# Optimization experiments

Measured on AMD Instinct MI355X. Metric: run time of the kernel, lower is better.

The kernel has to match this reference:

```python
import jax, jax.numpy as jnp
import numpy as np

# dims: B=1, T=2048 (prefill), dim=3072, Hq=32, Hkv=8, D=128, S=max_seq_len=4096

def _rotate_interleave(x):
    # (-x1, x0, -x3, x2, ...) pairwise rotation on last dim
    x = x.reshape(x.shape[:-1] + (-1, 2))
    x = jnp.stack((-x[..., 1], x[..., 0]), axis=-1)
    return x.reshape(x.shape[:-2] + (-1,))


def setup_inputs() -> dict:
    key = jax.random.key(0)
    ks = jax.random.split(key, 8)
    B, T, DIM, HQ, HKV, HD, S = 1, 2048, 3072, 32, 8, 128, 4096
    x = jax.random.normal(ks[0], (B, T, DIM), jnp.float32)
    wq = jax.random.normal(ks[1], (HQ * HD, DIM), jnp.float32) * 0.02
    wk = jax.random.normal(ks[2], (HKV * HD, DIM), jnp.float32) * 0.02
    wv = jax.random.normal(ks[3], (HKV * HD, DIM), jnp.float32) * 0.02
    wo = jax.random.normal(ks[4], (DIM, HQ * HD), jnp.float32) * 0.02
    freqs_cos = jax.random.uniform(ks[5], (T, HD), jnp.float32)
    freqs_sin = jax.random.uniform(ks[6], (T, HD), jnp.float32)
    input_pos = jnp.zeros((1,), jnp.int32)
    k_cache = jnp.zeros((1, S, HKV, HD), jnp.float32)
    v_cache = jnp.zeros((1, S, HKV, HD), jnp.float32)
    return {"x": x, "wq": wq, "wk": wk, "wv": wv, "wo": wo,
            "freqs_cos": freqs_cos, "freqs_sin": freqs_sin,
            "k_cache": k_cache, "v_cache": v_cache, "input_pos": input_pos}


def reference(x, wq, wk, wv, wo, freqs_cos, freqs_sin, k_cache, v_cache, input_pos):
    B, T, _ = x.shape
    HQ, HKV, HD = 32, 8, 128
    q = (x @ wq.T).reshape(B, T, HQ, HD)
    k = (x @ wk.T).reshape(B, T, HKV, HD)
    v = (x @ wv.T).reshape(B, T, HKV, HD)
    # interleaved RoPE (computed in fp32 as in apply_rotary_emb)
    fc = freqs_cos[None, :, None, :]
    fs = freqs_sin[None, :, None, :]
    q = q * fc + _rotate_interleave(q) * fs
    k = k * fc + _rotate_interleave(k) * fs
    # KV-cache update at start_pos (torch.ops.llama.update_cache)
    sp = input_pos[0]
    k_all = jax.lax.dynamic_update_slice(k_cache, k, (0, sp, 0, 0))  # [1,S,HKV,HD]
    v_all = jax.lax.dynamic_update_slice(v_cache, v, (0, sp, 0, 0))
    S = k_all.shape[1]
    # GQA: expand kv heads to match q heads (head h -> kv head h // rep)
    rep = HQ // HKV
    kr = jnp.repeat(k_all, rep, axis=2)  # [1,S,HQ,HD]
    vr = jnp.repeat(v_all, rep, axis=2)
    scale = 1.0 / np.sqrt(HD).astype(np.float32)
    scores = jnp.einsum('bthd,bshd->bhts', q, kr) * scale  # [B,HQ,T,S]
    # causal mask relative to start_pos (custom_sdpa is_causal=True path)
    qpos = sp + jnp.arange(T)
    kpos = jnp.arange(S)
    mask = kpos[None, :] <= qpos[:, None]                   # [T,S]
    scores = jnp.where(mask[None, None], scores, jnp.float32(-1e30))
    attn = jax.nn.softmax(scores, axis=-1)
    y = jnp.einsum('bhts,bshd->bthd', attn, vr).reshape(B, T, HQ * HD)
    return y @ wo.T
```

## Files before the change

### kernel.cpp

```cpp
#include <hip/hip_runtime.h>
#include <hip/hip_bf16.h>
#include <stdint.h>

typedef float f32x4 __attribute__((ext_vector_type(4)));
typedef short s16x8 __attribute__((ext_vector_type(8)));
typedef short s16x4 __attribute__((ext_vector_type(4)));
typedef unsigned short u16x2 __attribute__((ext_vector_type(2)));
typedef unsigned short u16x4 __attribute__((ext_vector_type(4)));

#define AS1 __attribute__((address_space(1)))
#define AS3 __attribute__((address_space(3)))

static constexpr int T_    = 2048;
static constexpr int DIM_  = 3072;
static constexpr int HQ_   = 32;
static constexpr int HKV_  = 8;
static constexpr int HD_   = 128;
static constexpr int S_    = 4096;
static constexpr int NQKV_ = HQ_ * HD_ + 2 * HKV_ * HD_;

__device__ __forceinline__ unsigned short f2b(float f) {
  return __builtin_bit_cast(unsigned short, __float2bfloat16(f));
}
__device__ __forceinline__ float b2f(unsigned short u) {
  return __bfloat162float(__builtin_bit_cast(__hip_bfloat16, u));
}
__device__ __forceinline__ float exp2a(float x) {
  float r; asm("v_exp_f32 %0, %1" : "=v"(r) : "v"(x)); return r;
}

__device__ __forceinline__ void gld_lds16(const void* g, void* l) {
  __builtin_amdgcn_global_load_lds((AS1 unsigned int*)(uintptr_t)g,
                                   (AS3 unsigned int*)l, 16, 0, 0);
}

#define FENCE() asm volatile("" ::: "memory")
#define BAR()   do { FENCE(); __builtin_amdgcn_s_barrier(); FENCE(); } while (0)
#define WAIT_VM(n)   asm volatile("s_waitcnt vmcnt(" #n ")" ::: "memory")
#define WAIT_LGKM(n) asm volatile("s_waitcnt lgkmcnt(" #n ")" ::: "memory")
#define SCHEDB()     __builtin_amdgcn_sched_barrier(0)

__global__ __launch_bounds__(256)
void k_cvt(const float* __restrict__ src, unsigned short* __restrict__ dst, int n4) {
  int i = blockIdx.x * 256 + threadIdx.x;
  if (i >= n4) return;
  float4 v = reinterpret_cast<const float4*>(src)[i];
  u16x4 o;
  o.x = f2b(v.x); o.y = f2b(v.y); o.z = f2b(v.z); o.w = f2b(v.w);
  reinterpret_cast<u16x4*>(dst)[i] = o;
}

__global__ __launch_bounds__(256)
void k_cvtW(const float* __restrict__ wq, const float* __restrict__ wk,
            const float* __restrict__ wv, unsigned short* __restrict__ dst) {
  int idx = blockIdx.x * 256 + threadIdx.x;
  if (idx >= 4718592) return;
  const float* src; int s;
  if (idx < 3145728)      { src = wq; s = idx; }
  else if (idx < 3932160) { src = wk; s = idx - 3145728; }
  else                    { src = wv; s = idx - 3932160; }
  float4 v = reinterpret_cast<const float4*>(src)[s];
  u16x4 o;
  o.x = f2b(v.x); o.y = f2b(v.y); o.z = f2b(v.z); o.w = f2b(v.w);
  reinterpret_cast<u16x4*>(dst)[idx] = o;
}

template<int BMT, bool OUT_BF16>
__global__ __launch_bounds__(512, 4)
void k_gemm192(const unsigned short* __restrict__ A,
               const unsigned short* __restrict__ B,
               void* __restrict__ Cout, int N, int K, int KT,
               int nbn, int xcdq) {
  constexpr int AROWS  = BMT / 64;
  constexpr int AFRAG  = BMT / 32;
  constexpr int LDSBUF = BMT * 128 + 24576;
  __shared__ char lds[2 * LDSBUF];
  const int bid = blockIdx.x;
  const int swz = (bid & 7) * xcdq + (bid >> 3);
  const int bm  = swz / nbn, bn = swz % nbn;
  const int tid = threadIdx.x, lane = tid & 63, wid = tid >> 6;
  const int wm  = wid >> 2, wn = wid & 3;
  const int r16 = lane & 15, q4 = lane >> 4;

  const unsigned short* Ag = A + (size_t)(bm * BMT) * K;
  const unsigned short* Bg = B + (size_t)(bn * 192) * K;

  const int srow = tid >> 3;
  const int scol = ((tid & 7) ^ (srow & 7)) * 8;

  f32x4 acc[AFRAG][3] = {};
  s16x8 af[AFRAG][2];

  auto stageA = [&](int c, int r, int t) {
    gld_lds16(Ag + (size_t)(r * 64 + srow) * K + t * 64 + scol,
              lds + c * LDSBUF + r * 8192 + tid * 16);
  };
  auto stageB = [&](int c, int r, int t) {
    gld_lds16(Bg + (size_t)(r * 64 + srow) * K + t * 64 + scol,
              lds + c * LDSBUF + BMT * 128 + r * 8192 + tid * 16);
  };
  auto readA = [&](int c) {
    #pragma unroll
    for (int i = 0; i < AFRAG; ++i) {
      const int arow = wm * (BMT / 2) + i * 16 + r16;
      #pragma unroll
      for (int kk = 0; kk < 2; ++kk)
        af[i][kk] = *(const s16x8*)(lds + c * LDSBUF + arow * 128 +
                                    (((kk * 4 + q4) ^ (arow & 7)) << 4));
    }
  };
  auto readB = [&](s16x8 (&dst)[2], int c, int j) {
    const int brow = wn * 48 + j * 16 + r16;
    #pragma unroll
    for (int kk = 0; kk < 2; ++kk)
      dst[kk] = *(const s16x8*)(lds + c * LDSBUF + BMT * 128 + brow * 128 +
                                (((kk * 4 + q4) ^ (brow & 7)) << 4));
  };

#define MFMA8(BF, J)                                                           \
  __builtin_amdgcn_s_setprio(1);                                               \
  _Pragma("unroll")                                                            \
  for (int i_ = 0; i_ < AFRAG; ++i_) {                                         \
    _Pragma("unroll")                                                          \
    for (int kk_ = 0; kk_ < 2; ++kk_)                                          \
      acc[i_][J] = __builtin_amdgcn_mfma_f32_16x16x32_bf16(                    \
          af[i_][kk_], BF[kk_], acc[i_][J], 0, 0, 0);                          \
  }                                                                            \
  __builtin_amdgcn_s_setprio(0);

  #pragma unroll
  for (int r = 0; r < AROWS; ++r) stageA(0, r, 0);
  stageB(0, 0, 0); stageB(0, 1, 0); stageB(0, 2, 0);
  WAIT_VM(0);
  BAR();

  for (int t = 0; t < KT; ++t) {
    const int c = t & 1;
    const bool hn = (t + 1 < KT);
    {
      s16x8 bfc[2];
      readA(c); readB(bfc, c, 0);
      if (hn) {
        stageA(c ^ 1, 0, t + 1);
        if constexpr (BMT == 128) stageA(c ^ 1, 1, t + 1);
        else                      stageB(c ^ 1, 0, t + 1);
      }
      BAR();
      WAIT_LGKM(0); SCHEDB();
      MFMA8(bfc, 0);
      BAR();
    }
    {
      s16x8 bfc[2];
      readB(bfc, c, 1);
      if (hn) {
        if constexpr (BMT == 128) { stageB(c ^ 1, 0, t + 1); stageB(c ^ 1, 1, t + 1); }
        else                      { stageB(c ^ 1, 1, t + 1); }
      }
      BAR();
      WAIT_LGKM(0); SCHEDB();
      MFMA8(bfc, 1);
      BAR();
    }
    {
      s16x8 bfc[2];
      readB(bfc, c, 2);
      if (hn) stageB(c ^ 1, 2, t + 1);
      BAR();
      WAIT_LGKM(0); SCHEDB();
      MFMA8(bfc, 2);
      if (hn) { WAIT_VM(0); }
      BAR();
    }
  }
#undef MFMA8

  #pragma unroll
  for (int i = 0; i < AFRAG; ++i) {
    const int row = bm * BMT + wm * (BMT / 2) + i * 16 + q4 * 4;
    #pragma unroll
    for (int j = 0; j < 3; ++j) {
      const int col = bn * 192 + wn * 48 + j * 16 + r16;
      if constexpr (OUT_BF16) {
        unsigned short* C = (unsigned short*)Cout;
        #pragma unroll
        for (int rr = 0; rr < 4; ++rr)
          C[(size_t)(row + rr) * N + col] = f2b(acc[i][j][rr]);
      } else {
        float* C = (float*)Cout;
        #pragma unroll
        for (int rr = 0; rr < 4; ++rr)
          C[(size_t)(row + rr) * N + col] = acc[i][j][rr];
      }
    }
  }
}

__global__ __launch_bounds__(256)
void k_prep(const unsigned short* __restrict__ qkv,
            const float* __restrict__ fc, const float* __restrict__ fs,
            const float* __restrict__ kc, const float* __restrict__ vc,
            unsigned short* __restrict__ Qr, unsigned short* __restrict__ Kall,
            unsigned short* __restrict__ VT, const int* __restrict__ ipos) {
  __shared__ unsigned short lds[64][136];
  const int b = blockIdx.x, tid = threadIdx.x;

  if (b < 4096) {
    int idx = b * 256 + tid;
    int t   = idx >> 9;
    int rem = idx & 511;
    int h   = rem >> 4;
    int c8  = (rem & 15) << 3;
    s16x8 xv = *(const s16x8*)(qkv + (size_t)t * NQKV_ + h * HD_ + c8);
    float4 ca = *(const float4*)(fc + t * HD_ + c8);
    float4 cb = *(const float4*)(fc + t * HD_ + c8 + 4);
    float4 sa = *(const float4*)(fs + t * HD_ + c8);
    float4 sb = *(const float4*)(fs + t * HD_ + c8 + 4);
    float cc[8] = {ca.x, ca.y, ca.z, ca.w, cb.x, cb.y, cb.z, cb.w};
    float ss[8] = {sa.x, sa.y, sa.z, sa.w, sb.x, sb.y, sb.z, sb.w};
    s16x8 o;
    #pragma unroll
    for (int i = 0; i < 4; ++i) {
      float x0 = b2f((unsigned short)xv[2 * i]);
      float x1 = b2f((unsigned short)xv[2 * i + 1]);
      o[2 * i]     = (short)f2b(x0 * cc[2 * i]     - x1 * ss[2 * i]);
      o[2 * i + 1] = (short)f2b(x1 * cc[2 * i + 1] + x0 * ss[2 * i + 1]);
    }
    *(s16x8*)(Qr + ((size_t)h * T_ + t) * HD_ + c8) = o;

  } else if (b < 5120) {
    int idx = (b - 4096) * 256 + tid;
    int t   = idx >> 7;
    int rem = idx & 127;
    int hk  = rem >> 4;
    int c8  = (rem & 15) << 3;
    int sp  = ipos[0];
    s16x8 xv = *(const s16x8*)(qkv + (size_t)t * NQKV_ + HQ_ * HD_ + hk * HD_ + c8);
    float4 ca = *(const float4*)(fc + t * HD_ + c8);
    float4 cb = *(const float4*)(fc + t * HD_ + c8 + 4);
    float4 sa = *(const float4*)(fs + t * HD_ + c8);
    float4 sb = *(const float4*)(fs + t * HD_ + c8 + 4);
    float cc[8] = {ca.x, ca.y, ca.z, ca.w, cb.x, cb.y, cb.z, cb.w};
    float ss[8] = {sa.x, sa.y, sa.z, sa.w, sb.x, sb.y, sb.z, sb.w};
    s16x8 o;
    #pragma unroll
    for (int i = 0; i < 4; ++i) {
      float x0 = b2f((unsigned short)xv[2 * i]);
      float x1 = b2f((unsigned short)xv[2 * i + 1]);
      o[2 * i]     = (short)f2b(x0 * cc[2 * i]     - x1 * ss[2 * i]);
      o[2 * i + 1] = (short)f2b(x1 * cc[2 * i + 1] + x0 * ss[2 * i + 1]);
    }
    *(s16x8*)(Kall + ((size_t)hk * S_ + sp + t) * HD_ + c8) = o;

  } else if (b < 5376) {
    int bb = b - 5120;
    int hk = bb >> 5;
    int tt = bb & 31;
    int sp = ipos[0];
    #pragma unroll
    for (int p = 0; p < 4; ++p) {
      int e   = p * 256 + tid;
      int tr  = e >> 4;
      int col = (e & 15) << 3;
      *reinterpret_cast<s16x8*>(&lds[tr][col]) =
          *reinterpret_cast<const s16x8*>(&qkv[(size_t)(tt * 64 + tr) * NQKV_ +
                                               (HQ_ + HKV_) * HD_ + hk * HD_ + col]);
    }
    __syncthreads();
    #pragma unroll
    for (int p = 0; p < 32; ++p) {
      int e = p * 256 + tid;
      int d = e >> 6;
      int t = e & 63;
      VT[((size_t)hk * HD_ + d) * S_ + sp + tt * 64 + t] = lds[t][d];
    }

  } else {
    int sp = ipos[0];
    int total = sp * HKV_ * HD_;
    for (int idx = (b - 5376) * 256 + tid; idx < total; idx += 256 * 256) {
      int s   = idx >> 10;
      int rem = idx & 1023;
      int hk  = rem >> 7;
      int d   = rem & 127;
      Kall[((size_t)hk * S_ + s) * HD_ + d] = f2b(kc[((size_t)s * HKV_ + hk) * HD_ + d]);
      VT[((size_t)hk * HD_ + d) * S_ + s]   = f2b(vc[((size_t)s * HKV_ + hk) * HD_ + d]);
    }
  }
}

__global__ __launch_bounds__(256, 2)
void k_attn(const unsigned short* __restrict__ Qr,
            const unsigned short* __restrict__ Kall,
            const unsigned short* __restrict__ VT,
            unsigned short* __restrict__ Y,
            const int* __restrict__ ipos) {
  constexpr int QB = 64, KB = 64;
  __shared__ char lds[65536];
  const int bid  = blockIdx.x;
  const int hk   = bid & 7;
  const int j2   = bid >> 3;
  const int h    = hk * 4 + (j2 & 3);
  const int qt   = 31 - (j2 >> 2);
  const int tid  = threadIdx.x, lane = tid & 63, wave = tid >> 6;
  const int r16  = lane & 15, q4 = lane >> 4;
  const int vx   = r16 & 7;
  const float NEG_INF = -__builtin_inff();
  const float MINIT   = -1.0e30f;

  const int sp = ipos[0];
  const int qbase = qt * QB + wave * 16;
  const unsigned short* Kbase = Kall + (size_t)hk * S_ * HD_;
  const unsigned short* Vbase = VT + (size_t)hk * HD_ * S_;

  s16x8 qf[4];
  const unsigned short* qp = Qr + ((size_t)h * T_ + qbase + r16) * HD_;
  #pragma unroll
  for (int ki = 0; ki < 4; ++ki)
    qf[ki] = *reinterpret_cast<const s16x8*>(qp + ki * 32 + q4 * 8);
  SCHEDB(); WAIT_VM(0); SCHEDB();

  auto stage = [&](int c, int jt) {
    #pragma unroll
    for (int p = 0; p < 4; ++p) {
      int e  = p * 256 + tid;
      int kr = e >> 4;
      int ks = (e & 15) ^ (kr & 7);
      gld_lds16(Kbase + (size_t)(jt * KB + kr) * HD_ + ks * 8,
                lds + c * 16384 + e * 16);
    }
    #pragma unroll
    for (int p = 0; p < 4; ++p) {
      int e  = p * 256 + tid;
      int vd = e >> 3;
      int vs = (e & 7) ^ (vd & 7);
      gld_lds16(Vbase + (size_t)vd * S_ + jt * KB + vs * 8,
                lds + 32768 + c * 16384 + e * 16);
    }
  };

  f32x4 o[8] = {};
  float m = MINIT, l = 0.f;
  const int qpos = sp + qbase + r16;
  const int qpos_wave_max = sp + qbase + 15;
  int jmax = (sp + qt * QB + QB - 1) >> 6;
  if (jmax > S_ / KB - 1) jmax = S_ / KB - 1;
  const float scale2 = 0.12751744416312068f;

  stage(0, 0);

  for (int j = 0; j <= jmax; ++j) {
    const int c = j & 1;
    if (j < jmax) { stage(c ^ 1, j + 1); WAIT_VM(8); }
    else         { WAIT_VM(0); }
    BAR();

    const bool active = (j * KB <= qpos_wave_max);
    if (active) {
      const char* kb = lds + c * 16384;
      const char* vb = lds + 32768 + c * 16384;
      f32x4 sfr[4];
      #pragma unroll
      for (int fn = 0; fn < 4; ++fn) {
        sfr[fn] = f32x4{0.f, 0.f, 0.f, 0.f};
        #pragma unroll
        for (int ki = 0; ki < 4; ++ki) {
          s16x8 kf = *(const s16x8*)(kb + (fn * 16 + r16) * 256 +
                                     (((ki * 4 + q4) ^ vx) << 4));
          sfr[fn] = __builtin_amdgcn_mfma_f32_16x16x32_bf16(kf, qf[ki], sfr[fn], 0, 0, 0);
        }
      }
      float p[16];
      const bool needMask = (j * KB + KB - 1) > (sp + qbase);
      if (needMask) {
        const int kbp = j * KB + q4 * 4;
        #pragma unroll
        for (int fn = 0; fn < 4; ++fn)
          #pragma unroll
          for (int r = 0; r < 4; ++r)
            p[fn * 4 + r] = (kbp + fn * 16 + r <= qpos) ? sfr[fn][r] * scale2 : NEG_INF;
      } else {
        #pragma unroll
        for (int fn = 0; fn < 4; ++fn)
          #pragma unroll
          for (int r = 0; r < 4; ++r)
            p[fn * 4 + r] = sfr[fn][r] * scale2;
      }
      float pmax = p[0];
      #pragma unroll
      for (int i = 1; i < 16; ++i) pmax = fmaxf(pmax, p[i]);
      pmax = fmaxf(pmax, __shfl_xor(pmax, 16));
      pmax = fmaxf(pmax, __shfl_xor(pmax, 32));
      if (!__all(pmax <= m + 8.0f)) {
        float mn = fmaxf(m, pmax);
        float alpha = exp2a(m - mn);
        m = mn; l *= alpha;
        #pragma unroll
        for (int r = 0; r < 4; ++r) {
          float aq = __shfl(alpha, q4 * 4 + r);
          #pragma unroll
          for (int db = 0; db < 8; ++db) o[db][r] *= aq;
        }
      }
      float rs = 0.f;
      #pragma unroll
      for (int i = 0; i < 16; ++i) { p[i] = exp2a(p[i] - m); rs += p[i]; }
      rs += __shfl_xor(rs, 16); rs += __shfl_xor(rs, 32);
      l += rs;
      s16x8 pf[2];
      #pragma unroll
      for (int w = 0; w < 2; ++w)
        #pragma unroll
        for (int i = 0; i < 8; ++i)
          pf[w][i] = (short)f2b(p[w * 8 + i]);
      const int voff = (q4 & 1) * 8;
      const int sbase = q4 >> 1;
      #pragma unroll
      for (int w = 0; w < 2; ++w) {
        #pragma unroll
        for (int db = 0; db < 8; ++db) {
          const char* vr = vb + (db * 16 + r16) * 128 + voff;
          s16x4 va = *(const s16x4*)(vr + (((w * 4 + sbase) ^ vx) << 4));
          s16x4 vb2 = *(const s16x4*)(vr + (((w * 4 + 2 + sbase) ^ vx) << 4));
          s16x8 vf = __builtin_shufflevector(va, vb2, 0, 1, 2, 3, 4, 5, 6, 7);
          o[db] = __builtin_amdgcn_mfma_f32_16x16x32_bf16(pf[w], vf, o[db], 0, 0, 0);
        }
      }
    }
    BAR();
  }

  float rcpl = 1.0f / l;
  float rlq[4];
  #pragma unroll
  for (int r = 0; r < 4; ++r) rlq[r] = __shfl(rcpl, q4 * 4 + r);
  #pragma unroll
  for (int db = 0; db < 8; ++db)
    #pragma unroll
    for (int r = 0; r < 4; ++r) {
      int t = qt * QB + wave * 16 + q4 * 4 + r;
      int d = db * 16 + r16;
      Y[(size_t)t * (HQ_ * HD_) + h * HD_ + d] = f2b(o[db][r] * rlq[r]);
    }
}

extern "C" void kernel_launch(void* const* d_in, const int* in_sizes, int n_in,
                              void* d_out, int out_size, void* d_ws, size_t ws_size,
                              hipStream_t stream) {
  const float* x  = (const float*)d_in[0];
  const float* wq = (const float*)d_in[1];
  const float* wk = (const float*)d_in[2];
  const float* wv = (const float*)d_in[3];
  const float* wo = (const float*)d_in[4];
  const float* fc = (const float*)d_in[5];
  const float* fs = (const float*)d_in[6];
  const float* kc = (const float*)d_in[7];
  const float* vc = (const float*)d_in[8];
  const int* ipos = (const int*)d_in[9];

  char* ws = (char*)d_ws;
  unsigned short* xb   = (unsigned short*)(ws);
  unsigned short* wqkv = (unsigned short*)(ws + 12582912);
  unsigned short* qkv  = (unsigned short*)(ws + 50331648);
  unsigned short* Qr   = (unsigned short*)(ws + 75497472);
  unsigned short* Kall = (unsigned short*)(ws + 92274688);
  unsigned short* VT   = (unsigned short*)(ws + 100663296);
  unsigned short* wo_b = (unsigned short*)(ws);
  unsigned short* y    = qkv;

  k_cvt<<<6144, 256, 0, stream>>>(x, xb, 6291456 / 4);
  k_cvtW<<<18432, 256, 0, stream>>>(wq, wk, wv, wqkv);

  k_gemm192<128, true><<<512, 512, 0, stream>>>(xb, wqkv, qkv, NQKV_, DIM_, 48, 32, 64);

  k_cvt<<<12288, 256, 0, stream>>>(wo, wo_b, 12582912 / 4);

  k_prep<<<5632, 256, 0, stream>>>(qkv, fc, fs, kc, vc, Qr, Kall, VT, ipos);

  k_attn<<<1024, 256, 0, stream>>>(Qr, Kall, VT, y, ipos);

  k_gemm192<64, false><<<512, 512, 0, stream>>>(y, wo_b, d_out, DIM_, HQ_ * HD_, 64, 16, 64);
}
```

Baseline: 256.0 us.

## Merge GEMM k-step phases into one barrier, add MFMA priority in attention

The GEMM main loop drops its three barrier-separated sub-phases. Each k-step now issues all next-tile global stages up front, software-pipelines the B fragment LDS reads against the MFMAs with partial lgkm waits, and uses a single barrier per iteration. This cuts barrier stalls, at the cost of more registers and more memory traffic in flight at once. The attention kernel also wraps its QK and PV MFMA blocks in s_setprio and replaces the serial row-max chain with a tree reduction to shorten the dependency chain.

```diff
diff --git a/kernel.cpp b/kernel.cpp
--- a/kernel.cpp
+++ b/kernel.cpp
@@ -137,41 +137,24 @@
   for (int t = 0; t < KT; ++t) {
     const int c = t & 1;
     const bool hn = (t + 1 < KT);
-    {
-      s16x8 bfc[2];
-      readA(c); readB(bfc, c, 0);
-      if (hn) {
-        stageA(c ^ 1, 0, t + 1);
-        if constexpr (BMT == 128) stageA(c ^ 1, 1, t + 1);
-        else                      stageB(c ^ 1, 0, t + 1);
-      }
-      BAR();
-      WAIT_LGKM(0); SCHEDB();
-      MFMA8(bfc, 0);
-      BAR();
-    }
-    {
-      s16x8 bfc[2];
-      readB(bfc, c, 1);
-      if (hn) {
-        if constexpr (BMT == 128) { stageB(c ^ 1, 0, t + 1); stageB(c ^ 1, 1, t + 1); }
-        else                      { stageB(c ^ 1, 1, t + 1); }
-      }
-      BAR();
-      WAIT_LGKM(0); SCHEDB();
-      MFMA8(bfc, 1);
-      BAR();
-    }
-    {
-      s16x8 bfc[2];
-      readB(bfc, c, 2);
-      if (hn) stageB(c ^ 1, 2, t + 1);
-      BAR();
-      WAIT_LGKM(0); SCHEDB();
-      MFMA8(bfc, 2);
-      if (hn) { WAIT_VM(0); }
-      BAR();
-    }
+    s16x8 bf0[2], bf1[2], bf2[2];
+    readA(c);
+    readB(bf0, c, 0);
+    if (hn) {
+      #pragma unroll
+      for (int r = 0; r < AROWS; ++r) stageA(c ^ 1, r, t + 1);
+      stageB(c ^ 1, 0, t + 1); stageB(c ^ 1, 1, t + 1); stageB(c ^ 1, 2, t + 1);
+    }
+    readB(bf1, c, 1);
+    WAIT_LGKM(2); SCHEDB();
+    MFMA8(bf0, 0);
+    readB(bf2, c, 2);
+    WAIT_LGKM(2); SCHEDB();
+    MFMA8(bf1, 1);
+    WAIT_LGKM(0); SCHEDB();
+    MFMA8(bf2, 2);
+    if (hn) WAIT_VM(0);
+    BAR();
   }
 #undef MFMA8
 
@@ -360,6 +343,7 @@
       const char* kb = lds + c * 16384;
       const char* vb = lds + 32768 + c * 16384;
       f32x4 sfr[4];
+      __builtin_amdgcn_s_setprio(1);
       #pragma unroll
       for (int fn = 0; fn < 4; ++fn) {
         sfr[fn] = f32x4{0.f, 0.f, 0.f, 0.f};
@@ -370,6 +354,7 @@
           sfr[fn] = __builtin_amdgcn_mfma_f32_16x16x32_bf16(kf, qf[ki], sfr[fn], 0, 0, 0);
         }
       }
+      __builtin_amdgcn_s_setprio(0);
       float p[16];
       const bool needMask = (j * KB + KB - 1) > (sp + qbase);
       if (needMask) {
@@ -386,9 +371,13 @@
           for (int r = 0; r < 4; ++r)
             p[fn * 4 + r] = sfr[fn][r] * scale2;
       }
-      float pmax = p[0];
-      #pragma unroll
-      for (int i = 1; i < 16; ++i) pmax = fmaxf(pmax, p[i]);
+      float t0 = fmaxf(p[0], p[1]),  t1 = fmaxf(p[2], p[3]);
+      float t2 = fmaxf(p[4], p[5]),  t3 = fmaxf(p[6], p[7]);
+      float t4 = fmaxf(p[8], p[9]),  t5 = fmaxf(p[10], p[11]);
+      float t6 = fmaxf(p[12], p[13]), t7 = fmaxf(p[14], p[15]);
+      float u0 = fmaxf(t0, t1), u1 = fmaxf(t2, t3);
+      float u2 = fmaxf(t4, t5), u3 = fmaxf(t6, t7);
+      float pmax = fmaxf(fmaxf(u0, u1), fmaxf(u2, u3));
       pmax = fmaxf(pmax, __shfl_xor(pmax, 16));
       pmax = fmaxf(pmax, __shfl_xor(pmax, 32));
       if (!__all(pmax <= m + 8.0f)) {
@@ -415,6 +404,7 @@
           pf[w][i] = (short)f2b(p[w * 8 + i]);
       const int voff = (q4 & 1) * 8;
       const int sbase = q4 >> 1;
+      __builtin_amdgcn_s_setprio(1);
       #pragma unroll
       for (int w = 0; w < 2; ++w) {
         #pragma unroll
@@ -426,6 +416,7 @@
           o[db] = __builtin_amdgcn_mfma_f32_16x16x32_bf16(pf[w], vf, o[db], 0, 0, 0);
         }
       }
+      __builtin_amdgcn_s_setprio(0);
     }
     BAR();
   }
```

Result: faster. 250.6 us (-2.1%).
